# Kernel optimization log

Hardware: AMD Instinct MI355X
Metric: run time of the kernel (lower is better)

The kernel has to match this reference:

```python
import jax, jax.numpy as jnp
import numpy as np

K_NN = 10  # k in the source

def setup_inputs() -> dict:
    key = jax.random.key(0)
    k1, k2, k3, k4, k5 = jax.random.split(key, 5)
    bs, N, d, n_concepts, n_classes = 4096, 200000, 256, 32, 10
    return {
        "train_embedding": jax.random.normal(k1, (bs, d), dtype=jnp.float32),
        "train_embeddings": jax.random.normal(k2, (N, d), dtype=jnp.float32),
        # init_concept: uniform in [-0.5, 0.5]
        "concept": jax.random.uniform(k3, (d, n_concepts), dtype=jnp.float32, minval=-0.5, maxval=0.5),
        "W_hx": jax.random.normal(k4, (d, n_classes), dtype=jnp.float32) * 0.05,
        "b_hx": jax.random.normal(k5, (n_classes,), dtype=jnp.float32) * 0.05,
    }


def reference(train_embedding, train_embeddings, concept, W_hx, b_hx):
    # concept: [d, nc]; train_embeddings: [N, d]; train_embedding: [bs, d]
    n_concepts = concept.shape[1]

    def h_x(z):  # linear classifier standing in for h_x
        return z @ W_hx + b_hx

    gram = concept.T @ concept                                # [nc, nc]
    proj_matrix = concept @ jnp.linalg.inv(gram) @ concept.T  # [d, d]
    proj = train_embedding @ proj_matrix.T                    # (proj_matrix @ X^T)^T, [bs, d]
    y_pred = h_x(proj)
    orig_pred = h_x(train_embedding)

    # Batched cdist across all concepts (replaces the per-concept python loop):
    # dist[n, j] = || train_embeddings[n] - concept[:, j] ||
    x2 = jnp.sum(train_embeddings * train_embeddings, axis=1, keepdims=True)  # [N, 1]
    c2 = jnp.sum(concept * concept, axis=0)                                   # [nc]
    xc = train_embeddings @ concept                                           # [N, nc]
    dist = jnp.sqrt(jnp.maximum(x2 + c2 - 2.0 * xc, 0.0))                     # [N, nc]

    # top-k SMALLEST distances per concept
    _, knn_idx = jax.lax.top_k(-dist.T, K_NN)          # [nc, k]
    knn = train_embeddings[knn_idx]                    # [nc, k, d] gather

    # L_sparse_1: mean over concepts of sum(c * c_knn) / k
    dots = jnp.einsum("dj,jkd->j", concept, knn) / K_NN   # [nc]
    L_sparse_1_new = jnp.mean(dots)

    eye = jnp.eye(n_concepts, dtype=gram.dtype)
    L_sparse_2_new = jnp.mean(gram * (1.0 - eye))
    norm_metrics = jnp.mean(gram * eye)

    return (orig_pred, y_pred, L_sparse_1_new, L_sparse_2_new, norm_metrics)
```

## Files before the change

### kernel.cpp

```cpp
#include <hip/hip_runtime.h>
#include <cstdint>

#define D 256
#define NC 32
#define NCLS 10
#define KNN 10
#define KROWS 128
#define CTS 260
#define NPART 8

typedef float f32x4 __attribute__((ext_vector_type(4)));
typedef float f4v __attribute__((ext_vector_type(4)));
typedef short short8v __attribute__((ext_vector_type(8)));

__device__ __forceinline__ float wave_sum(float v) {
  #pragma unroll
  for (int off = 32; off; off >>= 1) v += __shfl_xor(v, off);
  return v;
}

__device__ __forceinline__ uint32_t fbits(float x) { return __builtin_bit_cast(uint32_t, x); }
__device__ __forceinline__ float bcast(uint32_t b) { return __builtin_bit_cast(float, b); }

__global__ __launch_bounds__(512, 4) void k_key(const float* __restrict__ X,
                                                const float* __restrict__ C,
                                                float* __restrict__ candK,
                                                int* __restrict__ candI,
                                                int N, int G) {
  __shared__ uint4 shm[2048];
  int t = threadIdx.x;
  int lane = t & 63;
  int wvu = __builtin_amdgcn_readfirstlane(t >> 6);
  int rowbase = blockIdx.x * KROWS;

  #pragma unroll
  for (int e0 = 0; e0 < 1024; e0 += 512) {
    int e = e0 + t;
    int q = e >> 6, l = e & 63;
    int tile = q >> 3, ksq = q & 7;
    int col = tile * 16 + (l & 15), kg = (l >> 4) & 3;
    uint32_t h[8], lo[8];
    #pragma unroll
    for (int i = 0; i < 8; ++i) {
      int k = ksq * 32 + kg * 8 + i;
      float x = C[(size_t)k * NC + col];
      uint32_t hb = fbits(x) & 0xFFFF0000u;
      h[i] = hb >> 16;
      lo[i] = fbits(x - bcast(hb)) >> 16;
    }
    shm[e] = make_uint4((h[1] << 16) | h[0], (h[3] << 16) | h[2],
                        (h[5] << 16) | h[4], (h[7] << 16) | h[6]);
    shm[1024 + e] = make_uint4((lo[1] << 16) | lo[0], (lo[3] << 16) | lo[2],
                               (lo[5] << 16) | lo[4], (lo[7] << 16) | lo[6]);
  }
  __syncthreads();

  int r16 = lane & 15;
  int grow = rowbase + wvu * 16 + r16; if (grow >= N) grow = N - 1;
  const float* xp = X + (size_t)grow * D + ((lane >> 4) * 8);

  f32x4 aH0, aM0, aH1, aM1;
  #pragma unroll
  for (int i = 0; i < 4; ++i) { aH0[i] = 0.f; aM0[i] = 0.f; aH1[i] = 0.f; aM1[i] = 0.f; }
  float x2 = 0.f;

  #pragma unroll
  for (int ks = 0; ks < 8; ++ks) {
    f4v xa = __builtin_nontemporal_load(reinterpret_cast<const f4v*>(xp + ks * 32));
    f4v xb = __builtin_nontemporal_load(reinterpret_cast<const f4v*>(xp + ks * 32 + 4));
    float xs[8] = {xa[0], xa[1], xa[2], xa[3], xb[0], xb[1], xb[2], xb[3]};
    uint32_t hp[4], lp[4];
    #pragma unroll
    for (int p = 0; p < 4; ++p) {
      float x0 = xs[2 * p], x1 = xs[2 * p + 1];
      x2 = fmaf(x0, x0, x2); x2 = fmaf(x1, x1, x2);
      uint32_t h0 = fbits(x0) & 0xFFFF0000u, h1 = fbits(x1) & 0xFFFF0000u;
      hp[p] = h1 | (h0 >> 16);
      float r0 = x0 - bcast(h0), r1 = x1 - bcast(h1);
      lp[p] = (fbits(r1) & 0xFFFF0000u) | (fbits(r0) >> 16);
    }
    short8v xh = __builtin_bit_cast(short8v, make_uint4(hp[0], hp[1], hp[2], hp[3]));
    short8v xl = __builtin_bit_cast(short8v, make_uint4(lp[0], lp[1], lp[2], lp[3]));
    short8v b0h = __builtin_bit_cast(short8v, shm[ks * 64 + lane]);
    short8v b1h = __builtin_bit_cast(short8v, shm[(8 + ks) * 64 + lane]);
    short8v b0l = __builtin_bit_cast(short8v, shm[1024 + ks * 64 + lane]);
    short8v b1l = __builtin_bit_cast(short8v, shm[1024 + (8 + ks) * 64 + lane]);
    aH0 = __builtin_amdgcn_mfma_f32_16x16x32_bf16(xh, b0h, aH0, 0, 0, 0);
    aM0 = __builtin_amdgcn_mfma_f32_16x16x32_bf16(xh, b0l, aM0, 0, 0, 0);
    aM0 = __builtin_amdgcn_mfma_f32_16x16x32_bf16(xl, b0h, aM0, 0, 0, 0);
    aH1 = __builtin_amdgcn_mfma_f32_16x16x32_bf16(xh, b1h, aH1, 0, 0, 0);
    aM1 = __builtin_amdgcn_mfma_f32_16x16x32_bf16(xh, b1l, aM1, 0, 0, 0);
    aM1 = __builtin_amdgcn_mfma_f32_16x16x32_bf16(xl, b1h, aM1, 0, 0, 0);
  }

  x2 += __shfl_xor(x2, 16);
  x2 += __shfl_xor(x2, 32);

  __syncthreads();
  float* klb = reinterpret_cast<float*>(shm);
  #pragma unroll
  for (int i = 0; i < 4; ++i) {
    int m = (lane >> 4) * 4 + i;
    float x2m = __shfl(x2, m);
    int rowl = wvu * 16 + m;
    klb[rowl * 33 + r16]      = fmaf(-2.f, aH0[i] + aM0[i], x2m);
    klb[rowl * 33 + 16 + r16] = fmaf(-2.f, aH1[i] + aM1[i], x2m);
  }
  __syncthreads();

  {
    int c = t >> 4, sub = t & 15;
    const float INF = 3.4e38f;
    float bk[8]; int bi[8];
    #pragma unroll
    for (int q = 0; q < 8; ++q) { bk[q] = INF; bi[q] = 0x7fffffff; }
    #pragma unroll
    for (int rr = 0; rr < 8; ++rr) {
      int rowl = sub * 8 + rr;
      int gi = rowbase + rowl;
      float v = (gi < N) ? klb[rowl * 33 + c] : INF;
      float cv = v; int ci = gi;
      #pragma unroll
      for (int q = 0; q < 8; ++q) {
        bool take = (cv < bk[q]) || (cv == bk[q] && ci < bi[q]);
        if (take) {
          float tf = bk[q]; bk[q] = cv; cv = tf;
          int ti = bi[q]; bi[q] = ci; ci = ti;
        }
      }
    }
    #pragma unroll
    for (int r = 0; r < KNN; ++r) {
      float mv = bk[0]; int mgi = bi[0];
      #pragma unroll
      for (int off = 1; off < 16; off <<= 1) {
        float ov = __shfl_xor(mv, off); int oi = __shfl_xor(mgi, off);
        if (ov < mv || (ov == mv && oi < mgi)) { mv = ov; mgi = oi; }
      }
      bool won = (bk[0] == mv) && (bi[0] == mgi);
      #pragma unroll
      for (int q = 0; q < 7; ++q) {
        bk[q] = won ? bk[q + 1] : bk[q];
        bi[q] = won ? bi[q + 1] : bi[q];
      }
      if (won) { bk[7] = INF; bi[7] = 0x7fffffff; }
      if (sub == 0) {
        candK[((size_t)c * G + blockIdx.x) * KNN + r] = mv;
        candI[((size_t)c * G + blockIdx.x) * KNN + r] = mgi;
      }
    }
  }
}

#define AUGW (NC + NCLS)
__global__ __launch_bounds__(1024) void k_gramsolve(const float* __restrict__ C,
                                                    const float* __restrict__ W,
                                                    float* __restrict__ T2,
                                                    float* __restrict__ out, int bs) {
  __shared__ float T[(NC + NCLS) * CTS];
  __shared__ float aug[NC * AUGW];
  __shared__ float Ssh[NC * NCLS];
  int tid = threadIdx.x;

  const float4* C4 = (const float4*)C;
  for (int s = tid; s < 2048; s += 1024) {
    float4 v = C4[s];
    int d = s >> 3, c0 = (s & 7) * 4;
    T[(c0 + 0) * CTS + d] = v.x; T[(c0 + 1) * CTS + d] = v.y;
    T[(c0 + 2) * CTS + d] = v.z; T[(c0 + 3) * CTS + d] = v.w;
  }
  const float2* W2 = (const float2*)W;
  for (int s = tid; s < 1280; s += 1024) {
    float2 v = W2[s];
    int d = s / 5, c0 = (s % 5) * 2;
    T[(NC + c0) * CTS + d] = v.x; T[(NC + c0 + 1) * CTS + d] = v.y;
  }
  __syncthreads();

  int lane = tid & 63, wv = tid >> 6;
  #pragma unroll
  for (int half = 0; half < 2; ++half) {
    int i = wv + half * 16;
    if (lane < AUGW) {
      const float4* ri = (const float4*)&T[i * CTS];
      const float4* rj = (const float4*)&T[lane * CTS];
      float acc = 0.f;
      #pragma unroll 8
      for (int d4 = 0; d4 < 64; ++d4) {
        float4 a = ri[d4], b = rj[d4];
        acc += a.x * b.x + a.y * b.y + a.z * b.z + a.w * b.w;
      }
      aug[i * AUGW + lane] = acc;
    }
  }
  __syncthreads();

  if (tid < NC) {
    int l2 = tid;
    float row[AUGW];
    #pragma unroll
    for (int c = 0; c < AUGW; ++c) row[c] = aug[l2 * AUGW + c];

    float rsum = 0.f;
    #pragma unroll
    for (int c = 0; c < NC; ++c) rsum += row[c];
    float diag = row[l2];
    #pragma unroll
    for (int off = 16; off; off >>= 1) {
      rsum += __shfl_xor(rsum, off);
      diag += __shfl_xor(diag, off);
    }
    if (l2 == 0) {
      out[(size_t)2 * bs * NCLS + 1] = (rsum - diag) / (float)(NC * NC);
      out[(size_t)2 * bs * NCLS + 2] = diag / (float)(NC * NC);
      out[(size_t)2 * bs * NCLS] = 0.f;
    }

    for (int k = 0; k < NC; ++k) {
      float prow[AUGW];
      #pragma unroll
      for (int c = 0; c < AUGW; ++c) prow[c] = __shfl(row[c], k);
      float pinv = 1.0f / prow[k];
      float f = row[k] * pinv;
      if (l2 == k) {
        #pragma unroll
        for (int c = 0; c < AUGW; ++c) row[c] *= pinv;
      } else {
        #pragma unroll
        for (int c = 0; c < AUGW; ++c) row[c] -= f * prow[c];
      }
    }
    #pragma unroll
    for (int c = 0; c < NCLS; ++c) Ssh[l2 * NCLS + c] = row[NC + c];
  }
  __syncthreads();

  for (int e = tid; e < D * NCLS; e += 1024) {
    int d = e / NCLS, cls = e % NCLS;
    float acc = 0.f;
    #pragma unroll
    for (int c = 0; c < NC; ++c) acc += T[c * CTS + d] * Ssh[c * NCLS + cls];
    T2[e] = acc;
  }
}

__global__ __launch_bounds__(256) void k_pred(const float* __restrict__ X,
                                              const float* __restrict__ W,
                                              const float* __restrict__ T2,
                                              const float* __restrict__ bvec,
                                              float* __restrict__ out, int bs) {
  __shared__ float2 Ws2[1280];
  __shared__ float2 Ts2[1280];
  int t = threadIdx.x;
  const float2* W2 = (const float2*)W;
  const float2* T22 = (const float2*)T2;
  for (int s = t; s < 1280; s += 256) { Ws2[s] = W2[s]; Ts2[s] = T22[s]; }
  __syncthreads();

  int r = blockIdx.x * 8 + (t >> 5);
  int q = t & 31;
  const float4* x4 = reinterpret_cast<const float4*>(X + (size_t)r * D);
  float4 xa = x4[q * 2], xb = x4[q * 2 + 1];

  float o[NCLS], y[NCLS];
  #pragma unroll
  for (int c = 0; c < NCLS; ++c) { o[c] = 0.f; y[c] = 0.f; }

  #pragma unroll
  for (int i = 0; i < 8; ++i) {
    int d = q * 8 + i;
    float xd = (i < 4) ? reinterpret_cast<const float*>(&xa)[i]
                       : reinterpret_cast<const float*>(&xb)[i - 4];
    #pragma unroll
    for (int j = 0; j < 5; ++j) {
      float2 wv = Ws2[d * 5 + j];
      float2 tv = Ts2[d * 5 + j];
      o[j * 2 + 0] += xd * wv.x; o[j * 2 + 1] += xd * wv.y;
      y[j * 2 + 0] += xd * tv.x; y[j * 2 + 1] += xd * tv.y;
    }
  }
  #pragma unroll
  for (int off = 1; off < 32; off <<= 1) {
    #pragma unroll
    for (int c = 0; c < NCLS; ++c) {
      o[c] += __shfl_xor(o[c], off);
      y[c] += __shfl_xor(y[c], off);
    }
  }
  if (q < NCLS) {
    float b = bvec[q];
    out[(size_t)r * NCLS + q] = o[q] + b;
    out[(size_t)bs * NCLS + (size_t)r * NCLS + q] = y[q] + b;
  }
}

__device__ __forceinline__ void block_merge_top10(float* bk, int* bi, int tid,
                                                  float* sk, int* si,
                                                  float* wv_, int* wi_,
                                                  float* outK, int* outI) {
  const float INF = 3.4e38f;
  #pragma unroll
  for (int q = 0; q < KNN; ++q) { sk[tid * KNN + q] = bk[q]; si[tid * KNN + q] = bi[q]; }
  __syncthreads();
  int p = 0;
  int lane = tid & 63, wv = tid >> 6;
  for (int rr = 0; rr < KNN; ++rr) {
    float myv = (p < KNN) ? sk[tid * KNN + p] : INF;
    int mygi = (p < KNN) ? si[tid * KNN + p] : 0x7fffffff;
    float hv = myv; int hgi = mygi;
    #pragma unroll
    for (int off = 32; off; off >>= 1) {
      float ov = __shfl_xor(hv, off); int oi = __shfl_xor(hgi, off);
      if (ov < hv || (ov == hv && oi < hgi)) { hv = ov; hgi = oi; }
    }
    if (lane == 0) { wv_[wv] = hv; wi_[wv] = hgi; }
    __syncthreads();
    float bv = wv_[0]; int bgi = wi_[0];
    #pragma unroll
    for (int w = 1; w < 4; ++w) {
      if (wv_[w] < bv || (wv_[w] == bv && wi_[w] < bgi)) { bv = wv_[w]; bgi = wi_[w]; }
    }
    if (p < KNN && myv == bv && mygi == bgi) p++;
    if (tid == 0) { outK[rr] = bv; outI[rr] = bgi; }
    __syncthreads();
  }
}

__global__ __launch_bounds__(256) void k_fmerge(const float* __restrict__ candK,
                                                const int* __restrict__ candI,
                                                float* __restrict__ c2K,
                                                int* __restrict__ c2I, int G) {
  int j = blockIdx.y, part = blockIdx.x, tid = threadIdx.x;
  int M = G * KNN;
  int chunk = (M + NPART - 1) / NPART;
  int lo = part * chunk;
  int hi = lo + chunk; if (hi > M) hi = M;
  const float INF = 3.4e38f;

  float bk[KNN]; int bi[KNN];
  #pragma unroll
  for (int q = 0; q < KNN; ++q) { bk[q] = INF; bi[q] = 0x7fffffff; }
  for (int e = lo + tid; e < hi; e += 256) {
    float v = candK[(size_t)j * M + e];
    int gi = candI[(size_t)j * M + e];
    if (v < bk[KNN - 1] || (v == bk[KNN - 1] && gi < bi[KNN - 1])) {
      float cv = v; int ci = gi;
      #pragma unroll
      for (int q = 0; q < KNN; ++q) {
        bool take = (cv < bk[q]) || (cv == bk[q] && ci < bi[q]);
        if (take) {
          float tf = bk[q]; bk[q] = cv; cv = tf;
          int ti = bi[q]; bi[q] = ci; ci = ti;
        }
      }
    }
  }

  __shared__ float sk[256 * KNN];
  __shared__ int si[256 * KNN];
  __shared__ float wv_[4]; __shared__ int wi_[4];
  block_merge_top10(bk, bi, tid, sk, si, wv_, wi_,
                    c2K + ((size_t)j * NPART + part) * KNN,
                    c2I + ((size_t)j * NPART + part) * KNN);
}

__global__ __launch_bounds__(256) void k_final2(const float* __restrict__ c2K,
                                                const int* __restrict__ c2I,
                                                const float* __restrict__ X,
                                                const float* __restrict__ Cc,
                                                float* __restrict__ out, int bs) {
  int j = blockIdx.x, tid = threadIdx.x;
  const int M2 = NPART * KNN;
  const float INF = 3.4e38f;

  float bk[KNN]; int bi[KNN];
  #pragma unroll
  for (int q = 0; q < KNN; ++q) { bk[q] = INF; bi[q] = 0x7fffffff; }
  if (tid < M2) {
    bk[0] = c2K[(size_t)j * M2 + tid];
    bi[0] = c2I[(size_t)j * M2 + tid];
  }

  __shared__ float sk[256 * KNN];
  __shared__ int si[256 * KNN];
  __shared__ float wv_[4]; __shared__ int wi_[4];
  __shared__ float topK[KNN]; __shared__ int topIdx[KNN];
  block_merge_top10(bk, bi, tid, sk, si, wv_, wi_, topK, topIdx);

  int lane = tid & 63, wv = tid >> 6;
  float cj = Cc[tid * NC + j];
  float acc = 0.f;
  #pragma unroll
  for (int k = 0; k < KNN; ++k) acc += X[(size_t)topIdx[k] * D + tid] * cj;
  acc = wave_sum(acc);
  __shared__ float rsum[4];
  if (lane == 0) rsum[wv] = acc;
  __syncthreads();
  if (tid == 0)
    atomicAdd(out + (size_t)2 * bs * NCLS,
              (rsum[0] + rsum[1] + rsum[2] + rsum[3]) * (1.0f / (KNN * NC)));
}

extern "C" void kernel_launch(void* const* d_in, const int* in_sizes, int n_in,
                              void* d_out, int out_size, void* d_ws, size_t ws_size,
                              hipStream_t stream) {
  const float* Xb = (const float*)d_in[0];
  const float* XN = (const float*)d_in[1];
  const float* C  = (const float*)d_in[2];
  const float* W  = (const float*)d_in[3];
  const float* bv = (const float*)d_in[4];
  float* out = (float*)d_out;

  int bs = in_sizes[0] / D;
  int N  = in_sizes[1] / D;
  int G  = (N + KROWS - 1) / KROWS;

  float* w = (float*)d_ws;
  size_t offT2   = 0;
  size_t offC2K  = 2560;
  size_t offC2I  = offC2K + NC * NPART * KNN;
  size_t offCK   = offC2I + NC * NPART * KNN;
  size_t offCI   = offCK + (size_t)NC * G * KNN;

  float* T2    = w + offT2;
  float* c2K   = w + offC2K;
  int*   c2I   = (int*)(w + offC2I);
  float* candK = w + offCK;
  int*   candI = (int*)(w + offCI);

  k_key<<<dim3(G), dim3(512), 0, stream>>>(XN, C, candK, candI, N, G);
  k_gramsolve<<<dim3(1), dim3(1024), 0, stream>>>(C, W, T2, out, bs);
  k_pred<<<dim3(bs / 8), dim3(256), 0, stream>>>(Xb, W, T2, bv, out, bs);
  k_fmerge<<<dim3(NPART, NC), dim3(256), 0, stream>>>(candK, candI, c2K, c2I, G);
  k_final2<<<dim3(NC), dim3(256), 0, stream>>>(c2K, c2I, XN, C, out, bs);
}
```

Before: 146.2 us.

## Split k_key K-dimension across two waves per row group and prefetch X rows

Doubles k_key's block to 1024 threads so each 16-row group is handled by two waves, each covering half of the 256-wide dimension. Partial MFMA results and squared norms are combined through shared memory with an extra barrier. All X loads for a wave are issued up front, before the concept matrix is staged into shared memory, so global latency overlaps the bf16 split setup. The change trades more threads per block, extra LDS traffic and synchronization, and half the threads idling during top-k, for more memory-level parallelism.

```diff
diff --git a/kernel.cpp b/kernel.cpp
--- a/kernel.cpp
+++ b/kernel.cpp
@@ -22,27 +22,39 @@
 __device__ __forceinline__ uint32_t fbits(float x) { return __builtin_bit_cast(uint32_t, x); }
 __device__ __forceinline__ float bcast(uint32_t b) { return __builtin_bit_cast(float, b); }
 
-__global__ __launch_bounds__(512, 4) void k_key(const float* __restrict__ X,
-                                                const float* __restrict__ C,
-                                                float* __restrict__ candK,
-                                                int* __restrict__ candI,
-                                                int N, int G) {
+__global__ __launch_bounds__(1024, 2) void k_key(const float* __restrict__ X,
+                                                 const float* __restrict__ C,
+                                                 float* __restrict__ candK,
+                                                 int* __restrict__ candI,
+                                                 int N, int G) {
   __shared__ uint4 shm[2048];
   int t = threadIdx.x;
   int lane = t & 63;
   int wvu = __builtin_amdgcn_readfirstlane(t >> 6);
+  int rg = wvu >> 1, kh = wvu & 1;
   int rowbase = blockIdx.x * KROWS;
 
-  #pragma unroll
-  for (int e0 = 0; e0 < 1024; e0 += 512) {
-    int e = e0 + t;
+  int r16 = lane & 15, kg = lane >> 4;
+  int grow = rowbase + rg * 16 + r16; if (grow >= N) grow = N - 1;
+  const float* xp = X + (size_t)grow * D + kh * 128 + kg * 8;
+
+  f4v xr[8];
+  #pragma unroll
+  for (int ksl = 0; ksl < 4; ++ksl) {
+    xr[2 * ksl]     = __builtin_nontemporal_load(reinterpret_cast<const f4v*>(xp + ksl * 32));
+    xr[2 * ksl + 1] = __builtin_nontemporal_load(reinterpret_cast<const f4v*>(xp + ksl * 32 + 4));
+  }
+  __builtin_amdgcn_sched_barrier(0);
+
+  {
+    int e = t;
     int q = e >> 6, l = e & 63;
     int tile = q >> 3, ksq = q & 7;
-    int col = tile * 16 + (l & 15), kg = (l >> 4) & 3;
+    int col = tile * 16 + (l & 15), kgf = (l >> 4) & 3;
     uint32_t h[8], lo[8];
     #pragma unroll
     for (int i = 0; i < 8; ++i) {
-      int k = ksq * 32 + kg * 8 + i;
+      int k = ksq * 32 + kgf * 8 + i;
       float x = C[(size_t)k * NC + col];
       uint32_t hb = fbits(x) & 0xFFFF0000u;
       h[i] = hb >> 16;
@@ -55,19 +67,15 @@
   }
   __syncthreads();
 
-  int r16 = lane & 15;
-  int grow = rowbase + wvu * 16 + r16; if (grow >= N) grow = N - 1;
-  const float* xp = X + (size_t)grow * D + ((lane >> 4) * 8);
-
   f32x4 aH0, aM0, aH1, aM1;
   #pragma unroll
   for (int i = 0; i < 4; ++i) { aH0[i] = 0.f; aM0[i] = 0.f; aH1[i] = 0.f; aM1[i] = 0.f; }
   float x2 = 0.f;
 
   #pragma unroll
-  for (int ks = 0; ks < 8; ++ks) {
-    f4v xa = __builtin_nontemporal_load(reinterpret_cast<const f4v*>(xp + ks * 32));
-    f4v xb = __builtin_nontemporal_load(reinterpret_cast<const f4v*>(xp + ks * 32 + 4));
+  for (int ksl = 0; ksl < 4; ++ksl) {
+    int ks = kh * 4 + ksl;
+    f4v xa = xr[2 * ksl], xb = xr[2 * ksl + 1];
     float xs[8] = {xa[0], xa[1], xa[2], xa[3], xb[0], xb[1], xb[2], xb[3]};
     uint32_t hp[4], lp[4];
     #pragma unroll
@@ -98,17 +106,31 @@
 
   __syncthreads();
   float* klb = reinterpret_cast<float*>(shm);
-  #pragma unroll
-  for (int i = 0; i < 4; ++i) {
-    int m = (lane >> 4) * 4 + i;
-    float x2m = __shfl(x2, m);
-    int rowl = wvu * 16 + m;
-    klb[rowl * 33 + r16]      = fmaf(-2.f, aH0[i] + aM0[i], x2m);
-    klb[rowl * 33 + 16 + r16] = fmaf(-2.f, aH1[i] + aM1[i], x2m);
-  }
-  __syncthreads();
-
-  {
+
+  if (kh == 1) {
+    #pragma unroll
+    for (int i = 0; i < 4; ++i) {
+      int m = kg * 4 + i;
+      int rowl = rg * 16 + m;
+      klb[rowl * 33 + r16]      = -2.f * (aH0[i] + aM0[i]);
+      klb[rowl * 33 + 16 + r16] = -2.f * (aH1[i] + aM1[i]);
+    }
+    if (kg == 0) klb[(rg * 16 + r16) * 33 + 32] = x2;
+  }
+  __syncthreads();
+  if (kh == 0) {
+    #pragma unroll
+    for (int i = 0; i < 4; ++i) {
+      int m = kg * 4 + i;
+      int rowl = rg * 16 + m;
+      float x2t = __shfl(x2, m) + klb[rowl * 33 + 32];
+      klb[rowl * 33 + r16]      += fmaf(-2.f, aH0[i] + aM0[i], x2t);
+      klb[rowl * 33 + 16 + r16] += fmaf(-2.f, aH1[i] + aM1[i], x2t);
+    }
+  }
+  __syncthreads();
+
+  if (t < 512) {
     int c = t >> 4, sub = t & 15;
     const float INF = 3.4e38f;
     float bk[8]; int bi[8];
@@ -428,7 +450,7 @@
   float* candK = w + offCK;
   int*   candI = (int*)(w + offCI);
 
-  k_key<<<dim3(G), dim3(512), 0, stream>>>(XN, C, candK, candI, N, G);
+  k_key<<<dim3(G), dim3(1024), 0, stream>>>(XN, C, candK, candI, N, G);
   k_gramsolve<<<dim3(1), dim3(1024), 0, stream>>>(C, W, T2, out, bs);
   k_pred<<<dim3(bs / 8), dim3(256), 0, stream>>>(Xb, W, T2, bv, out, bs);
   k_fmerge<<<dim3(NPART, NC), dim3(256), 0, stream>>>(candK, candI, c2K, c2I, G);
```

New measurement: 199.9 us. 36.7% more time.

## Fuse gram solve into key kernel and merge pred with first top-k merge

Applied to the files above, without the earlier changes.

The single-block gram/solve work becomes an extra block of the main distance/top-k kernel, and the prediction kernel and the partial top-k merge kernel are combined into one launch that dispatches on block index. This cuts the launch count from five to three and lets the small serial gram solve overlap with the large distance pass instead of running alone. In exchange the gram block now runs with 512 threads and a scalar, non-vectorised inner loop, and the combined kernels use a shared LDS footprint sized for the larger role.

```diff
diff --git a/kernel.cpp b/kernel.cpp
--- a/kernel.cpp
+++ b/kernel.cpp
@@ -6,8 +6,8 @@
 #define NCLS 10
 #define KNN 10
 #define KROWS 128
-#define CTS 260
 #define NPART 8
+#define PB 512
 
 typedef float f32x4 __attribute__((ext_vector_type(4)));
 typedef float f4v __attribute__((ext_vector_type(4)));
@@ -22,13 +22,103 @@
 __device__ __forceinline__ uint32_t fbits(float x) { return __builtin_bit_cast(uint32_t, x); }
 __device__ __forceinline__ float bcast(uint32_t b) { return __builtin_bit_cast(float, b); }
 
-__global__ __launch_bounds__(512, 4) void k_key(const float* __restrict__ X,
-                                                const float* __restrict__ C,
-                                                float* __restrict__ candK,
-                                                int* __restrict__ candI,
-                                                int N, int G) {
+#define AUGW (NC + NCLS)
+
+__global__ __launch_bounds__(512, 4) void k_main(const float* __restrict__ X,
+                                                 const float* __restrict__ C,
+                                                 const float* __restrict__ W,
+                                                 float* __restrict__ candK,
+                                                 int* __restrict__ candI,
+                                                 float* __restrict__ T2,
+                                                 float* __restrict__ out,
+                                                 int N, int G, int bs) {
   __shared__ uint4 shm[2048];
   int t = threadIdx.x;
+
+  if (blockIdx.x == (unsigned)G) {
+    float* Cf = reinterpret_cast<float*>(shm);
+    {
+      const float4* C4g = (const float4*)C;
+      float4* Cf4 = (float4*)Cf;
+      for (int s = t; s < 2048; s += 512) Cf4[s] = C4g[s];
+    }
+    __syncthreads();
+
+    int lane = t & 63, wv8 = t >> 6;
+    float augv[4];
+    #pragma unroll
+    for (int h = 0; h < 4; ++h) {
+      int i = wv8 + h * 8;
+      float acc = 0.f;
+      if (lane < AUGW) {
+        for (int d = 0; d < D; ++d) {
+          float ci = Cf[d * NC + i];
+          float bj = (lane < NC) ? Cf[d * NC + lane] : W[(size_t)d * NCLS + (lane - NC)];
+          acc = fmaf(ci, bj, acc);
+        }
+      }
+      augv[h] = acc;
+    }
+    __syncthreads();
+    float* augL = Cf;
+    float* Ssh = Cf + 1400;
+    #pragma unroll
+    for (int h = 0; h < 4; ++h) {
+      int i = wv8 + h * 8;
+      if (lane < AUGW) augL[i * AUGW + lane] = augv[h];
+    }
+    __syncthreads();
+
+    if (t < NC) {
+      int l2 = t;
+      float row[AUGW];
+      #pragma unroll
+      for (int c = 0; c < AUGW; ++c) row[c] = augL[l2 * AUGW + c];
+
+      float rsum = 0.f;
+      #pragma unroll
+      for (int c = 0; c < NC; ++c) rsum += row[c];
+      float diag = row[l2];
+      #pragma unroll
+      for (int off = 16; off; off >>= 1) {
+        rsum += __shfl_xor(rsum, off);
+        diag += __shfl_xor(diag, off);
+      }
+      if (l2 == 0) {
+        out[(size_t)2 * bs * NCLS + 1] = (rsum - diag) / (float)(NC * NC);
+        out[(size_t)2 * bs * NCLS + 2] = diag / (float)(NC * NC);
+        out[(size_t)2 * bs * NCLS] = 0.f;
+      }
+
+      for (int k = 0; k < NC; ++k) {
+        float prow[AUGW];
+        #pragma unroll
+        for (int c = 0; c < AUGW; ++c) prow[c] = __shfl(row[c], k);
+        float pinv = 1.0f / prow[k];
+        float f = row[k] * pinv;
+        if (l2 == k) {
+          #pragma unroll
+          for (int c = 0; c < AUGW; ++c) row[c] *= pinv;
+        } else {
+          #pragma unroll
+          for (int c = 0; c < AUGW; ++c) row[c] -= f * prow[c];
+        }
+      }
+      #pragma unroll
+      for (int c = 0; c < NCLS; ++c) Ssh[l2 * NCLS + c] = row[NC + c];
+    }
+    __syncthreads();
+
+    for (int e = t; e < D * NCLS; e += 512) {
+      int d = e / NCLS, cls = e % NCLS;
+      float acc = 0.f;
+      #pragma unroll
+      for (int c = 0; c < NC; ++c) acc = fmaf(C[(size_t)d * NC + c], Ssh[c * NCLS + cls], acc);
+      T2[e] = acc;
+    }
+    return;
+  }
+
   int lane = t & 63;
   int wvu = __builtin_amdgcn_readfirstlane(t >> 6);
   int rowbase = blockIdx.x * KROWS;
@@ -152,148 +242,6 @@
   }
 }
 
-#define AUGW (NC + NCLS)
-__global__ __launch_bounds__(1024) void k_gramsolve(const float* __restrict__ C,
-                                                    const float* __restrict__ W,
-                                                    float* __restrict__ T2,
-                                                    float* __restrict__ out, int bs) {
-  __shared__ float T[(NC + NCLS) * CTS];
-  __shared__ float aug[NC * AUGW];
-  __shared__ float Ssh[NC * NCLS];
-  int tid = threadIdx.x;
-
-  const float4* C4 = (const float4*)C;
-  for (int s = tid; s < 2048; s += 1024) {
-    float4 v = C4[s];
-    int d = s >> 3, c0 = (s & 7) * 4;
-    T[(c0 + 0) * CTS + d] = v.x; T[(c0 + 1) * CTS + d] = v.y;
-    T[(c0 + 2) * CTS + d] = v.z; T[(c0 + 3) * CTS + d] = v.w;
-  }
-  const float2* W2 = (const float2*)W;
-  for (int s = tid; s < 1280; s += 1024) {
-    float2 v = W2[s];
-    int d = s / 5, c0 = (s % 5) * 2;
-    T[(NC + c0) * CTS + d] = v.x; T[(NC + c0 + 1) * CTS + d] = v.y;
-  }
-  __syncthreads();
-
-  int lane = tid & 63, wv = tid >> 6;
-  #pragma unroll
-  for (int half = 0; half < 2; ++half) {
-    int i = wv + half * 16;
-    if (lane < AUGW) {
-      const float4* ri = (const float4*)&T[i * CTS];
-      const float4* rj = (const float4*)&T[lane * CTS];
-      float acc = 0.f;
-      #pragma unroll 8
-      for (int d4 = 0; d4 < 64; ++d4) {
-        float4 a = ri[d4], b = rj[d4];
-        acc += a.x * b.x + a.y * b.y + a.z * b.z + a.w * b.w;
-      }
-      aug[i * AUGW + lane] = acc;
-    }
-  }
-  __syncthreads();
-
-  if (tid < NC) {
-    int l2 = tid;
-    float row[AUGW];
-    #pragma unroll
-    for (int c = 0; c < AUGW; ++c) row[c] = aug[l2 * AUGW + c];
-
-    float rsum = 0.f;
-    #pragma unroll
-    for (int c = 0; c < NC; ++c) rsum += row[c];
-    float diag = row[l2];
-    #pragma unroll
-    for (int off = 16; off; off >>= 1) {
-      rsum += __shfl_xor(rsum, off);
-      diag += __shfl_xor(diag, off);
-    }
-    if (l2 == 0) {
-      out[(size_t)2 * bs * NCLS + 1] = (rsum - diag) / (float)(NC * NC);
-      out[(size_t)2 * bs * NCLS + 2] = diag / (float)(NC * NC);
-      out[(size_t)2 * bs * NCLS] = 0.f;
-    }
-
-    for (int k = 0; k < NC; ++k) {
-      float prow[AUGW];
-      #pragma unroll
-      for (int c = 0; c < AUGW; ++c) prow[c] = __shfl(row[c], k);
-      float pinv = 1.0f / prow[k];
-      float f = row[k] * pinv;
-      if (l2 == k) {
-        #pragma unroll
-        for (int c = 0; c < AUGW; ++c) row[c] *= pinv;
-      } else {
-        #pragma unroll
-        for (int c = 0; c < AUGW; ++c) row[c] -= f * prow[c];
-      }
-    }
-    #pragma unroll
-    for (int c = 0; c < NCLS; ++c) Ssh[l2 * NCLS + c] = row[NC + c];
-  }
-  __syncthreads();
-
-  for (int e = tid; e < D * NCLS; e += 1024) {
-    int d = e / NCLS, cls = e % NCLS;
-    float acc = 0.f;
-    #pragma unroll
-    for (int c = 0; c < NC; ++c) acc += T[c * CTS + d] * Ssh[c * NCLS + cls];
-    T2[e] = acc;
-  }
-}
-
-__global__ __launch_bounds__(256) void k_pred(const float* __restrict__ X,
-                                              const float* __restrict__ W,
-                                              const float* __restrict__ T2,
-                                              const float* __restrict__ bvec,
-                                              float* __restrict__ out, int bs) {
-  __shared__ float2 Ws2[1280];
-  __shared__ float2 Ts2[1280];
-  int t = threadIdx.x;
-  const float2* W2 = (const float2*)W;
-  const float2* T22 = (const float2*)T2;
-  for (int s = t; s < 1280; s += 256) { Ws2[s] = W2[s]; Ts2[s] = T22[s]; }
-  __syncthreads();
-
-  int r = blockIdx.x * 8 + (t >> 5);
-  int q = t & 31;
-  const float4* x4 = reinterpret_cast<const float4*>(X + (size_t)r * D);
-  float4 xa = x4[q * 2], xb = x4[q * 2 + 1];
-
-  float o[NCLS], y[NCLS];
-  #pragma unroll
-  for (int c = 0; c < NCLS; ++c) { o[c] = 0.f; y[c] = 0.f; }
-
-  #pragma unroll
-  for (int i = 0; i < 8; ++i) {
-    int d = q * 8 + i;
-    float xd = (i < 4) ? reinterpret_cast<const float*>(&xa)[i]
-                       : reinterpret_cast<const float*>(&xb)[i - 4];
-    #pragma unroll
-    for (int j = 0; j < 5; ++j) {
-      float2 wv = Ws2[d * 5 + j];
-      float2 tv = Ts2[d * 5 + j];
-      o[j * 2 + 0] += xd * wv.x; o[j * 2 + 1] += xd * wv.y;
-      y[j * 2 + 0] += xd * tv.x; y[j * 2 + 1] += xd * tv.y;
-    }
-  }
-  #pragma unroll
-  for (int off = 1; off < 32; off <<= 1) {
-    #pragma unroll
-    for (int c = 0; c < NCLS; ++c) {
-      o[c] += __shfl_xor(o[c], off);
-      y[c] += __shfl_xor(y[c], off);
-    }
-  }
-  if (q < NCLS) {
-    float b = bvec[q];
-    out[(size_t)r * NCLS + q] = o[q] + b;
-    out[(size_t)bs * NCLS + (size_t)r * NCLS + q] = y[q] + b;
-  }
-}
-
 __device__ __forceinline__ void block_merge_top10(float* bk, int* bi, int tid,
                                                   float* sk, int* si,
                                                   float* wv_, int* wi_,
@@ -326,11 +274,66 @@
   }
 }
 
-__global__ __launch_bounds__(256) void k_fmerge(const float* __restrict__ candK,
-                                                const int* __restrict__ candI,
-                                                float* __restrict__ c2K,
-                                                int* __restrict__ c2I, int G) {
-  int j = blockIdx.y, part = blockIdx.x, tid = threadIdx.x;
+__global__ __launch_bounds__(256) void k_pf(const float* __restrict__ Xb,
+                                            const float* __restrict__ W,
+                                            const float* __restrict__ T2,
+                                            const float* __restrict__ bvec,
+                                            float* __restrict__ out,
+                                            const float* __restrict__ candK,
+                                            const int* __restrict__ candI,
+                                            float* __restrict__ c2K,
+                                            int* __restrict__ c2I, int G, int bs) {
+  __shared__ __align__(16) char smem[20800];
+  int t = threadIdx.x;
+
+  if (blockIdx.x < (unsigned)PB) {
+    float2* Ws2 = (float2*)smem;
+    float2* Ts2 = (float2*)(smem + 10240);
+    const float2* W2 = (const float2*)W;
+    const float2* T22 = (const float2*)T2;
+    for (int s = t; s < 1280; s += 256) { Ws2[s] = W2[s]; Ts2[s] = T22[s]; }
+    __syncthreads();
+
+    int r = blockIdx.x * 8 + (t >> 5);
+    int q = t & 31;
+    const float4* x4 = reinterpret_cast<const float4*>(Xb + (size_t)r * D);
+    float4 xa = x4[q * 2], xb = x4[q * 2 + 1];
+
+    float o[NCLS], y[NCLS];
+    #pragma unroll
+    for (int c = 0; c < NCLS; ++c) { o[c] = 0.f; y[c] = 0.f; }
+
+    #pragma unroll
+    for (int i = 0; i < 8; ++i) {
+      int d = q * 8 + i;
+      float xd = (i < 4) ? reinterpret_cast<const float*>(&xa)[i]
+                         : reinterpret_cast<const float*>(&xb)[i - 4];
+      #pragma unroll
+      for (int j = 0; j < 5; ++j) {
+        float2 wv = Ws2[d * 5 + j];
+        float2 tv = Ts2[d * 5 + j];
+        o[j * 2 + 0] += xd * wv.x; o[j * 2 + 1] += xd * wv.y;
+        y[j * 2 + 0] += xd * tv.x; y[j * 2 + 1] += xd * tv.y;
+      }
+    }
+    #pragma unroll
+    for (int off = 1; off < 32; off <<= 1) {
+      #pragma unroll
+      for (int c = 0; c < NCLS; ++c) {
+        o[c] += __shfl_xor(o[c], off);
+        y[c] += __shfl_xor(y[c], off);
+      }
+    }
+    if (q < NCLS) {
+      float b = bvec[q];
+      out[(size_t)r * NCLS + q] = o[q] + b;
+      out[(size_t)bs * NCLS + (size_t)r * NCLS + q] = y[q] + b;
+    }
+    return;
+  }
+
+  int bid = blockIdx.x - PB;
+  int part = bid % NPART, j = bid / NPART;
   int M = G * KNN;
   int chunk = (M + NPART - 1) / NPART;
   int lo = part * chunk;
@@ -340,7 +343,7 @@
   float bk[KNN]; int bi[KNN];
   #pragma unroll
   for (int q = 0; q < KNN; ++q) { bk[q] = INF; bi[q] = 0x7fffffff; }
-  for (int e = lo + tid; e < hi; e += 256) {
+  for (int e = lo + t; e < hi; e += 256) {
     float v = candK[(size_t)j * M + e];
     int gi = candI[(size_t)j * M + e];
     if (v < bk[KNN - 1] || (v == bk[KNN - 1] && gi < bi[KNN - 1])) {
@@ -356,10 +359,11 @@
     }
   }
 
-  __shared__ float sk[256 * KNN];
-  __shared__ int si[256 * KNN];
-  __shared__ float wv_[4]; __shared__ int wi_[4];
-  block_merge_top10(bk, bi, tid, sk, si, wv_, wi_,
+  float* sk = (float*)smem;
+  int* si = (int*)(smem + 10240);
+  float* wv_ = (float*)(smem + 20480);
+  int* wi_ = (int*)(smem + 20480 + 16);
+  block_merge_top10(bk, bi, t, sk, si, wv_, wi_,
                     c2K + ((size_t)j * NPART + part) * KNN,
                     c2I + ((size_t)j * NPART + part) * KNN);
 }
@@ -428,9 +432,8 @@
   float* candK = w + offCK;
   int*   candI = (int*)(w + offCI);
 
-  k_key<<<dim3(G), dim3(512), 0, stream>>>(XN, C, candK, candI, N, G);
-  k_gramsolve<<<dim3(1), dim3(1024), 0, stream>>>(C, W, T2, out, bs);
-  k_pred<<<dim3(bs / 8), dim3(256), 0, stream>>>(Xb, W, T2, bv, out, bs);
-  k_fmerge<<<dim3(NPART, NC), dim3(256), 0, stream>>>(candK, candI, c2K, c2I, G);
+  k_main<<<dim3(G + 1), dim3(512), 0, stream>>>(XN, C, W, candK, candI, T2, out, N, G, bs);
+  k_pf<<<dim3(PB + NPART * NC), dim3(256), 0, stream>>>(Xb, W, T2, bv, out,
+                                                        candK, candI, c2K, c2I, G, bs);
   k_final2<<<dim3(NC), dim3(256), 0, stream>>>(c2K, c2I, XN, C, out, bs);
 }
```

New measurement: 169.1 us. 15.6% more time.
